# Kernel tuning notes

Measured on AMD Instinct MI355X. Metric: run time of the kernel, lower is better.

The kernel has to match this reference:

```python
import jax, jax.numpy as jnp
import numpy as np

M, N, K = 4096, 8192, 4096


def setup_inputs() -> dict:
    key = jax.random.key(0)
    k1, k2, k3, k4 = jax.random.split(key, 4)
    a = jax.random.randint(k1, (M, K), 0, 127, dtype=jnp.int32)  # int8 activations
    b = jax.random.randint(k2, (N, K), 0, 127, dtype=jnp.int32)  # int8 weights (row-major [N,K])
    alpha_row = jax.random.uniform(k3, (M, 1), dtype=jnp.float16)  # per-row dequant scale
    alpha_col = jax.random.uniform(k4, (1, N), dtype=jnp.float16)  # per-col dequant scale
    return {"a": a, "b": b, "alpha_row": alpha_row, "alpha_col": alpha_col}


def reference(a, b, alpha_row, alpha_col):
    # x = a @ b.T in fp32 (int8 values upcast), then rescale by outer product of scales
    x = jnp.matmul(a.astype(jnp.float32), b.astype(jnp.float32).T)  # [M, N]
    scale = alpha_row.astype(jnp.float32) * alpha_col.astype(jnp.float32)  # [M, N] via broadcast
    out = x * scale
    return out.astype(jnp.float16)
```

## Files before the change

kernel.cpp:

```cpp
#include <hip/hip_runtime.h>
#include <cstdint>
#include <cstddef>

#define M_DIM 4096
#define N_DIM 8192
#define K_DIM 4096

typedef __attribute__((ext_vector_type(4))) int int4v;

__global__ void __launch_bounds__(256) pack_frag(const int* __restrict__ a,
                                                 const int* __restrict__ b,
                                                 unsigned char* __restrict__ pa,
                                                 unsigned char* __restrict__ pb) {
    size_t t = (size_t)blockIdx.x * 256 + threadIdx.x;
    const size_t NA = (size_t)(M_DIM / 16) * (K_DIM / 64) * 64;
    const int* __restrict__ src;
    unsigned char* __restrict__ dst;
    if (t < NA) {
        src = a; dst = pa;
    } else {
        src = b; dst = pb; t -= NA;
    }
    const int l = (int)(t & 63);
    const int s = (int)((t >> 6) & 63);
    const int p = (int)(t >> 12);
    const int* g = src + ((size_t)(16 * p + (l & 15))) * K_DIM + s * 64 + (l >> 4) * 16;
    const int4v* g4 = (const int4v*)g;
    int4v o;
#pragma unroll
    for (int q = 0; q < 4; ++q) {
        int4v v = g4[q];
        o[q] = (v[0] & 0xff) | ((v[1] & 0xff) << 8) | ((v[2] & 0xff) << 16) | (v[3] << 24);
    }
    ((int4v*)dst)[t] = o;
}

__device__ inline void async_copy16(const unsigned char* g, unsigned char* l) {
    __builtin_amdgcn_global_load_lds(
        (const __attribute__((address_space(1))) void*)g,
        (__attribute__((address_space(3))) void*)l,
        16, 0, 0);
}

__global__ void __launch_bounds__(256) gemm_i8(const unsigned char* __restrict__ Ap,
                                               const unsigned char* __restrict__ Bp,
                                               const _Float16* __restrict__ arow,
                                               const _Float16* __restrict__ acol,
                                               _Float16* __restrict__ Cout) {
    __shared__ __align__(16) unsigned char Bs[16384];

    const int tid  = threadIdx.x;
    const int lane = tid & 63;
    const int wave = tid >> 6;
    const int bn   = blockIdx.x;
    const int bm   = blockIdx.y;

    const int wm = (wave & 1) * 64;
    const int wn = (wave >> 1) * 64;

    const unsigned char* Abase =
        Ap + ((size_t)(bm * 8 + (wm >> 4))) * 65536 + lane * 16;

    const size_t Bblk = (size_t)bn * 8 * 65536;
    const unsigned char* bg[4];
    unsigned char* bl[4];
#pragma unroll
    for (int r = 0; r < 4; ++r) {
        const int offu = r * 4096 + wave * 1024;
        bg[r] = Bp + Bblk + (size_t)(offu >> 11) * 65536 + (offu & 2047) + lane * 16;
        bl[r] = Bs + offu;
    }

    const int bf_base = ((wn >> 4) << 11) + lane * 16;

    int4v acc[4][4];
#pragma unroll
    for (int i = 0; i < 4; ++i)
#pragma unroll
        for (int j = 0; j < 4; ++j) acc[i][j] = (int4v)0;

    for (int T = 0; T < K_DIM / 128; ++T) {
        const int gk = T * 2048;

        int4v af[2][4];
#pragma unroll
        for (int h = 0; h < 2; ++h)
#pragma unroll
            for (int i = 0; i < 4; ++i)
                af[h][i] = *(const int4v*)(Abase + (size_t)i * 65536 + gk + h * 1024);

#pragma unroll
        for (int r = 0; r < 4; ++r) async_copy16(bg[r] + gk, bl[r]);
        __syncthreads();

#pragma unroll
        for (int h = 0; h < 2; ++h) {
            int4v bf[4];
#pragma unroll
            for (int j = 0; j < 4; ++j)
                bf[j] = *(const int4v*)(Bs + bf_base + j * 2048 + h * 1024);
#pragma unroll
            for (int i = 0; i < 4; ++i)
#pragma unroll
                for (int j = 0; j < 4; ++j)
                    acc[i][j] = __builtin_amdgcn_mfma_i32_16x16x64_i8(af[h][i], bf[j],
                                                                      acc[i][j], 0, 0, 0);
        }
        __syncthreads();
    }

    const int gcol0 = bn * 128 + wn + (lane & 15);
    float ac4[4];
#pragma unroll
    for (int j = 0; j < 4; ++j) ac4[j] = (float)acol[gcol0 + j * 16];

    const size_t grow0 = (size_t)bm * 128 + wm + (lane >> 4) * 4;
#pragma unroll
    for (int i = 0; i < 4; ++i) {
#pragma unroll
        for (int r = 0; r < 4; ++r) {
            const size_t row = grow0 + i * 16 + r;
            const float ar = (float)arow[row];
            _Float16* outp = Cout + row * (size_t)N_DIM + gcol0;
#pragma unroll
            for (int j = 0; j < 4; ++j) {
                float v = (float)acc[i][j][r] * ar * ac4[j];
                outp[j * 16] = (_Float16)v;
            }
        }
    }
}

extern "C" void kernel_launch(void* const* d_in, const int* in_sizes, int n_in,
                              void* d_out, int out_size, void* d_ws, size_t ws_size,
                              hipStream_t stream) {
    const int* a = (const int*)d_in[0];
    const int* b = (const int*)d_in[1];
    const _Float16* ar = (const _Float16*)d_in[2];
    const _Float16* ac = (const _Float16*)d_in[3];
    _Float16* out = (_Float16*)d_out;

    unsigned char* pa = (unsigned char*)d_ws;
    unsigned char* pb = pa + (size_t)M_DIM * K_DIM;

    const size_t total_frag = (size_t)(M_DIM / 16 + N_DIM / 16) * (K_DIM / 64) * 64;
    pack_frag<<<(int)(total_frag / 256), 256, 0, stream>>>(a, b, pa, pb);

    dim3 grid(N_DIM / 128, M_DIM / 128);
    gemm_i8<<<grid, 256, 0, stream>>>(pa, pb, ar, ac, out);
}
```

Before: 392.8 us.

## Double-buffer B tile in LDS, enlarge M tile to 256, coalesce pack kernel

The GEMM now double-buffers the B tile in LDS, prefetching the next K-slice with async global-to-LDS copies while computing on the current one. This drops one barrier per iteration. Each wave computes 128x64 instead of 64x64, which doubles A-register reuse of B fragments, and the grid is swapped so blockIdx.x walks M. The pack kernel is rewritten so each thread reads one coalesced 16-byte group and scatters a 4-byte word into the fragment layout. The larger accumulator array raises register pressure, and launch_bounds(256,2) limits occupancy.

```diff
diff --git a/kernel.cpp b/kernel.cpp
--- a/kernel.cpp
+++ b/kernel.cpp
@@ -13,7 +13,7 @@
                                                  unsigned char* __restrict__ pa,
                                                  unsigned char* __restrict__ pb) {
     size_t t = (size_t)blockIdx.x * 256 + threadIdx.x;
-    const size_t NA = (size_t)(M_DIM / 16) * (K_DIM / 64) * 64;
+    const size_t NA = (size_t)M_DIM * (K_DIM / 4);
     const int* __restrict__ src;
     unsigned char* __restrict__ dst;
     if (t < NA) {
@@ -21,18 +21,14 @@
     } else {
         src = b; dst = pb; t -= NA;
     }
-    const int l = (int)(t & 63);
-    const int s = (int)((t >> 6) & 63);
-    const int p = (int)(t >> 12);
-    const int* g = src + ((size_t)(16 * p + (l & 15))) * K_DIM + s * 64 + (l >> 4) * 16;
-    const int4v* g4 = (const int4v*)g;
-    int4v o;
-#pragma unroll
-    for (int q = 0; q < 4; ++q) {
-        int4v v = g4[q];
-        o[q] = (v[0] & 0xff) | ((v[1] & 0xff) << 8) | ((v[2] & 0xff) << 16) | (v[3] << 24);
-    }
-    ((int4v*)dst)[t] = o;
+    const int r = (int)(t >> 10);
+    const int g = (int)(t & 1023);
+    int4v v = *(const int4v*)(src + (size_t)r * K_DIM + 4 * g);
+    const int w = (v[0] & 0xff) | ((v[1] & 0xff) << 8) | ((v[2] & 0xff) << 16) | (v[3] << 24);
+    const int p = r >> 4, lr = r & 15;
+    const int s = g >> 4, q = (g >> 2) & 3, bo = (g & 3) * 4;
+    const size_t off = ((size_t)(p * 64 + s) * 64 + (lr + 16 * q)) * 16 + bo;
+    *(int*)(dst + off) = w;
 }
 
 __device__ inline void async_copy16(const unsigned char* g, unsigned char* l) {
@@ -42,65 +38,71 @@
         16, 0, 0);
 }
 
-__global__ void __launch_bounds__(256) gemm_i8(const unsigned char* __restrict__ Ap,
-                                               const unsigned char* __restrict__ Bp,
-                                               const _Float16* __restrict__ arow,
-                                               const _Float16* __restrict__ acol,
-                                               _Float16* __restrict__ Cout) {
-    __shared__ __align__(16) unsigned char Bs[16384];
+__global__ void __launch_bounds__(256, 2) gemm_i8(const unsigned char* __restrict__ Ap,
+                                                  const unsigned char* __restrict__ Bp,
+                                                  const _Float16* __restrict__ arow,
+                                                  const _Float16* __restrict__ acol,
+                                                  _Float16* __restrict__ Cout) {
+    __shared__ __align__(16) unsigned char Bs[2 * 16384];
 
     const int tid  = threadIdx.x;
     const int lane = tid & 63;
     const int wave = tid >> 6;
-    const int bn   = blockIdx.x;
-    const int bm   = blockIdx.y;
+    const int bm   = blockIdx.x;
+    const int bn   = blockIdx.y;
 
-    const int wm = (wave & 1) * 64;
-    const int wn = (wave >> 1) * 64;
+    const int wmp = (wave & 1) * 8;
+    const int wnp = (wave >> 1) * 4;
 
-    const unsigned char* Abase =
-        Ap + ((size_t)(bm * 8 + (wm >> 4))) * 65536 + lane * 16;
+    const unsigned char* Abase = Ap + (size_t)(bm * 16 + wmp) * 65536 + lane * 16;
 
     const size_t Bblk = (size_t)bn * 8 * 65536;
     const unsigned char* bg[4];
-    unsigned char* bl[4];
+    int blo[4];
 #pragma unroll
     for (int r = 0; r < 4; ++r) {
         const int offu = r * 4096 + wave * 1024;
-        bg[r] = Bp + Bblk + (size_t)(offu >> 11) * 65536 + (offu & 2047) + lane * 16;
-        bl[r] = Bs + offu;
+        bg[r]  = Bp + Bblk + (size_t)(offu >> 11) * 65536 + (offu & 2047) + lane * 16;
+        blo[r] = offu;
     }
+    const int bf_base = wnp * 2048 + lane * 16;
 
-    const int bf_base = ((wn >> 4) << 11) + lane * 16;
-
-    int4v acc[4][4];
+    int4v acc[8][4];
 #pragma unroll
-    for (int i = 0; i < 4; ++i)
+    for (int i = 0; i < 8; ++i)
 #pragma unroll
         for (int j = 0; j < 4; ++j) acc[i][j] = (int4v)0;
 
+#pragma unroll
+    for (int r = 0; r < 4; ++r) async_copy16(bg[r], Bs + blo[r]);
+    __syncthreads();
+
     for (int T = 0; T < K_DIM / 128; ++T) {
-        const int gk = T * 2048;
+        const int cur = (T & 1) * 16384;
+        const int nxt = 16384 - cur;
+        const int gk  = T * 2048;
 
-        int4v af[2][4];
+        int4v af[2][8];
 #pragma unroll
         for (int h = 0; h < 2; ++h)
 #pragma unroll
-            for (int i = 0; i < 4; ++i)
+            for (int i = 0; i < 8; ++i)
                 af[h][i] = *(const int4v*)(Abase + (size_t)i * 65536 + gk + h * 1024);
 
+        if (T < K_DIM / 128 - 1) {
 #pragma unroll
-        for (int r = 0; r < 4; ++r) async_copy16(bg[r] + gk, bl[r]);
-        __syncthreads();
+            for (int r = 0; r < 4; ++r)
+                async_copy16(bg[r] + gk + 2048, Bs + nxt + blo[r]);
+        }
 
 #pragma unroll
         for (int h = 0; h < 2; ++h) {
             int4v bf[4];
 #pragma unroll
             for (int j = 0; j < 4; ++j)
-                bf[j] = *(const int4v*)(Bs + bf_base + j * 2048 + h * 1024);
+                bf[j] = *(const int4v*)(Bs + cur + bf_base + j * 2048 + h * 1024);
 #pragma unroll
-            for (int i = 0; i < 4; ++i)
+            for (int i = 0; i < 8; ++i)
 #pragma unroll
                 for (int j = 0; j < 4; ++j)
                     acc[i][j] = __builtin_amdgcn_mfma_i32_16x16x64_i8(af[h][i], bf[j],
@@ -109,14 +111,14 @@
         __syncthreads();
     }
 
-    const int gcol0 = bn * 128 + wn + (lane & 15);
+    const int gcol0 = bn * 128 + wnp * 16 + (lane & 15);
     float ac4[4];
 #pragma unroll
     for (int j = 0; j < 4; ++j) ac4[j] = (float)acol[gcol0 + j * 16];
 
-    const size_t grow0 = (size_t)bm * 128 + wm + (lane >> 4) * 4;
+    const size_t grow0 = (size_t)bm * 256 + wmp * 16 + (lane >> 4) * 4;
 #pragma unroll
-    for (int i = 0; i < 4; ++i) {
+    for (int i = 0; i < 8; ++i) {
 #pragma unroll
         for (int r = 0; r < 4; ++r) {
             const size_t row = grow0 + i * 16 + r;
@@ -143,9 +145,9 @@
     unsigned char* pa = (unsigned char*)d_ws;
     unsigned char* pb = pa + (size_t)M_DIM * K_DIM;
 
-    const size_t total_frag = (size_t)(M_DIM / 16 + N_DIM / 16) * (K_DIM / 64) * 64;
-    pack_frag<<<(int)(total_frag / 256), 256, 0, stream>>>(a, b, pa, pb);
+    const size_t groups = ((size_t)M_DIM + N_DIM) * (K_DIM / 4);
+    pack_frag<<<(int)(groups / 256), 256, 0, stream>>>(a, b, pa, pb);
 
-    dim3 grid(N_DIM / 128, M_DIM / 128);
+    dim3 grid(M_DIM / 256, N_DIM / 128);
     gemm_i8<<<grid, 256, 0, stream>>>(pa, pb, ar, ac, out);
 }
```

After: 428.0 us. 8.9% more time.

## Double-buffer B tiles in LDS and prefetch A fragments one K-step ahead

Applied to the files above, without the earlier changes.

Doubles the LDS buffer for B and splits the A fragment registers into ping-pong halves. Each iteration now issues the next tile's A loads and async B copies before computing on the current tile, so global latency can overlap with MFMA work. It also drops one barrier per iteration and adds a launch_bounds occupancy hint of 2. The cost is more registers for the second A buffer and twice the LDS, which may lower occupancy or cause spills.

```diff
diff --git a/kernel.cpp b/kernel.cpp
--- a/kernel.cpp
+++ b/kernel.cpp
@@ -42,12 +42,12 @@
         16, 0, 0);
 }
 
-__global__ void __launch_bounds__(256) gemm_i8(const unsigned char* __restrict__ Ap,
-                                               const unsigned char* __restrict__ Bp,
-                                               const _Float16* __restrict__ arow,
-                                               const _Float16* __restrict__ acol,
-                                               _Float16* __restrict__ Cout) {
-    __shared__ __align__(16) unsigned char Bs[16384];
+__global__ void __launch_bounds__(256, 2) gemm_i8(const unsigned char* __restrict__ Ap,
+                                                  const unsigned char* __restrict__ Bp,
+                                                  const _Float16* __restrict__ arow,
+                                                  const _Float16* __restrict__ acol,
+                                                  _Float16* __restrict__ Cout) {
+    __shared__ __align__(16) unsigned char Bs[2 * 16384];
 
     const int tid  = threadIdx.x;
     const int lane = tid & 63;
@@ -58,19 +58,17 @@
     const int wm = (wave & 1) * 64;
     const int wn = (wave >> 1) * 64;
 
-    const unsigned char* Abase =
-        Ap + ((size_t)(bm * 8 + (wm >> 4))) * 65536 + lane * 16;
+    const unsigned char* Abase = Ap + (size_t)(bm * 8 + (wm >> 4)) * 65536 + lane * 16;
 
     const size_t Bblk = (size_t)bn * 8 * 65536;
     const unsigned char* bg[4];
-    unsigned char* bl[4];
+    int blo[4];
 #pragma unroll
     for (int r = 0; r < 4; ++r) {
         const int offu = r * 4096 + wave * 1024;
-        bg[r] = Bp + Bblk + (size_t)(offu >> 11) * 65536 + (offu & 2047) + lane * 16;
-        bl[r] = Bs + offu;
+        bg[r]  = Bp + Bblk + (size_t)(offu >> 11) * 65536 + (offu & 2047) + lane * 16;
+        blo[r] = offu;
     }
-
     const int bf_base = ((wn >> 4) << 11) + lane * 16;
 
     int4v acc[4][4];
@@ -79,31 +77,47 @@
 #pragma unroll
         for (int j = 0; j < 4; ++j) acc[i][j] = (int4v)0;
 
-    for (int T = 0; T < K_DIM / 128; ++T) {
-        const int gk = T * 2048;
-
-        int4v af[2][4];
-#pragma unroll
-        for (int h = 0; h < 2; ++h)
-#pragma unroll
-            for (int i = 0; i < 4; ++i)
-                af[h][i] = *(const int4v*)(Abase + (size_t)i * 65536 + gk + h * 1024);
+    const int NT = K_DIM / 128;
+    int4v af[2][2][4];
 
 #pragma unroll
-        for (int r = 0; r < 4; ++r) async_copy16(bg[r] + gk, bl[r]);
-        __syncthreads();
+    for (int h = 0; h < 2; ++h)
+#pragma unroll
+        for (int i = 0; i < 4; ++i)
+            af[0][h][i] = *(const int4v*)(Abase + (size_t)i * 65536 + h * 1024);
+#pragma unroll
+    for (int r = 0; r < 4; ++r) async_copy16(bg[r], Bs + blo[r]);
+    __syncthreads();
 
+#pragma unroll 2
+    for (int T = 0; T < NT; ++T) {
+        const int pp = T & 1;
+        const int gkn = (T + 1) * 2048;
+
+        if (T + 1 < NT) {
+#pragma unroll
+            for (int h = 0; h < 2; ++h)
+#pragma unroll
+                for (int i = 0; i < 4; ++i)
+                    af[pp ^ 1][h][i] =
+                        *(const int4v*)(Abase + (size_t)i * 65536 + gkn + h * 1024);
+#pragma unroll
+            for (int r = 0; r < 4; ++r)
+                async_copy16(bg[r] + gkn, Bs + (pp ^ 1) * 16384 + blo[r]);
+        }
+
+        const unsigned char* Bcur = Bs + pp * 16384;
 #pragma unroll
         for (int h = 0; h < 2; ++h) {
             int4v bf[4];
 #pragma unroll
             for (int j = 0; j < 4; ++j)
-                bf[j] = *(const int4v*)(Bs + bf_base + j * 2048 + h * 1024);
+                bf[j] = *(const int4v*)(Bcur + bf_base + j * 2048 + h * 1024);
 #pragma unroll
             for (int i = 0; i < 4; ++i)
 #pragma unroll
                 for (int j = 0; j < 4; ++j)
-                    acc[i][j] = __builtin_amdgcn_mfma_i32_16x16x64_i8(af[h][i], bf[j],
+                    acc[i][j] = __builtin_amdgcn_mfma_i32_16x16x64_i8(af[pp][h][i], bf[j],
                                                                       acc[i][j], 0, 0, 0);
         }
         __syncthreads();
```

Measured after the change: 401.5 us. 2.2% more time.

## Use 256x256 block tiles with double-buffered LDS staging for A and B

Applied to the files above, without the earlier changes.

Grows the block tile from 128x128 to 256x256 with 512 threads (8 waves, each 64x128 output). A is now staged through LDS like B, and both use double-buffered async global-to-LDS copies so the next K-slice loads while the current one computes. The intent is to raise arithmetic intensity, cut redundant global traffic, and overlap memory with MFMA work. The cost is more accumulator registers (128 VGPRs of acc) and 64KB of LDS per block, which may limit occupancy. The grid drops to 512 blocks, which could leave the wave tail uneven across CUs.

```diff
diff --git a/kernel.cpp b/kernel.cpp
--- a/kernel.cpp
+++ b/kernel.cpp
@@ -42,12 +42,13 @@
         16, 0, 0);
 }
 
-__global__ void __launch_bounds__(256) gemm_i8(const unsigned char* __restrict__ Ap,
-                                               const unsigned char* __restrict__ Bp,
-                                               const _Float16* __restrict__ arow,
-                                               const _Float16* __restrict__ acol,
-                                               _Float16* __restrict__ Cout) {
-    __shared__ __align__(16) unsigned char Bs[16384];
+__global__ void __launch_bounds__(512, 2) gemm_i8(const unsigned char* __restrict__ Ap,
+                                                  const unsigned char* __restrict__ Bp,
+                                                  const _Float16* __restrict__ arow,
+                                                  const _Float16* __restrict__ acol,
+                                                  _Float16* __restrict__ Cout) {
+    __shared__ __align__(16) unsigned char As[2 * 16384];
+    __shared__ __align__(16) unsigned char Bs[2 * 16384];
 
     const int tid  = threadIdx.x;
     const int lane = tid & 63;
@@ -55,66 +56,76 @@
     const int bn   = blockIdx.x;
     const int bm   = blockIdx.y;
 
-    const int wm = (wave & 1) * 64;
-    const int wn = (wave >> 1) * 64;
+    const int pm0 = (wave & 3) * 4;
+    const int pn0 = (wave >> 2) * 8;
 
-    const unsigned char* Abase =
-        Ap + ((size_t)(bm * 8 + (wm >> 4))) * 65536 + lane * 16;
-
-    const size_t Bblk = (size_t)bn * 8 * 65536;
-    const unsigned char* bg[4];
-    unsigned char* bl[4];
+    const unsigned char* ag[2];
+    const unsigned char* bg[2];
+    int slo[2];
 #pragma unroll
-    for (int r = 0; r < 4; ++r) {
-        const int offu = r * 4096 + wave * 1024;
-        bg[r] = Bp + Bblk + (size_t)(offu >> 11) * 65536 + (offu & 2047) + lane * 16;
-        bl[r] = Bs + offu;
+    for (int r = 0; r < 2; ++r) {
+        const int p = 2 * wave + r;
+        ag[r]  = Ap + ((size_t)(bm * 16 + p) * 64) * 1024 + lane * 16;
+        bg[r]  = Bp + ((size_t)(bn * 16 + p) * 64) * 1024 + lane * 16;
+        slo[r] = p * 1024;
     }
 
-    const int bf_base = ((wn >> 4) << 11) + lane * 16;
+    const int a_off = pm0 * 1024 + lane * 16;
+    const int b_off = pn0 * 1024 + lane * 16;
 
-    int4v acc[4][4];
+    int4v acc[4][8];
 #pragma unroll
     for (int i = 0; i < 4; ++i)
 #pragma unroll
-        for (int j = 0; j < 4; ++j) acc[i][j] = (int4v)0;
+        for (int j = 0; j < 8; ++j) acc[i][j] = (int4v)0;
 
-    for (int T = 0; T < K_DIM / 128; ++T) {
-        const int gk = T * 2048;
-
-        int4v af[2][4];
-#pragma unroll
-        for (int h = 0; h < 2; ++h)
-#pragma unroll
-            for (int i = 0; i < 4; ++i)
-                af[h][i] = *(const int4v*)(Abase + (size_t)i * 65536 + gk + h * 1024);
+    const int NT = K_DIM / 64;
 
 #pragma unroll
-        for (int r = 0; r < 4; ++r) async_copy16(bg[r] + gk, bl[r]);
-        __syncthreads();
+    for (int r = 0; r < 2; ++r) {
+        async_copy16(ag[r], As + slo[r]);
+        async_copy16(bg[r], Bs + slo[r]);
+    }
+    __syncthreads();
+
+#pragma unroll 2
+    for (int T = 0; T < NT; ++T) {
+        const int cur = (T & 1) * 16384;
+        const int nxt = cur ^ 16384;
+
+        if (T + 1 < NT) {
+            const size_t gko = (size_t)(T + 1) * 1024;
+#pragma unroll
+            for (int r = 0; r < 2; ++r) {
+                async_copy16(ag[r] + gko, As + nxt + slo[r]);
+                async_copy16(bg[r] + gko, Bs + nxt + slo[r]);
+            }
+        }
+
+        int4v af[4], bf[8];
+#pragma unroll
+        for (int i = 0; i < 4; ++i)
+            af[i] = *(const int4v*)(As + cur + a_off + i * 1024);
+#pragma unroll
+        for (int j = 0; j < 8; ++j)
+            bf[j] = *(const int4v*)(Bs + cur + b_off + j * 1024);
 
 #pragma unroll
-        for (int h = 0; h < 2; ++h) {
-            int4v bf[4];
+        for (int i = 0; i < 4; ++i)
 #pragma unroll
-            for (int j = 0; j < 4; ++j)
-                bf[j] = *(const int4v*)(Bs + bf_base + j * 2048 + h * 1024);
-#pragma unroll
-            for (int i = 0; i < 4; ++i)
-#pragma unroll
-                for (int j = 0; j < 4; ++j)
-                    acc[i][j] = __builtin_amdgcn_mfma_i32_16x16x64_i8(af[h][i], bf[j],
-                                                                      acc[i][j], 0, 0, 0);
-        }
+            for (int j = 0; j < 8; ++j)
+                acc[i][j] = __builtin_amdgcn_mfma_i32_16x16x64_i8(af[i], bf[j],
+                                                                  acc[i][j], 0, 0, 0);
+
         __syncthreads();
     }
 
-    const int gcol0 = bn * 128 + wn + (lane & 15);
-    float ac4[4];
+    const int gcol0 = bn * 256 + pn0 * 16 + (lane & 15);
+    float ac8[8];
 #pragma unroll
-    for (int j = 0; j < 4; ++j) ac4[j] = (float)acol[gcol0 + j * 16];
+    for (int j = 0; j < 8; ++j) ac8[j] = (float)acol[gcol0 + j * 16];
 
-    const size_t grow0 = (size_t)bm * 128 + wm + (lane >> 4) * 4;
+    const size_t grow0 = (size_t)bm * 256 + pm0 * 16 + (lane >> 4) * 4;
 #pragma unroll
     for (int i = 0; i < 4; ++i) {
 #pragma unroll
@@ -123,8 +134,8 @@
             const float ar = (float)arow[row];
             _Float16* outp = Cout + row * (size_t)N_DIM + gcol0;
 #pragma unroll
-            for (int j = 0; j < 4; ++j) {
-                float v = (float)acc[i][j][r] * ar * ac4[j];
+            for (int j = 0; j < 8; ++j) {
+                float v = (float)acc[i][j][r] * ar * ac8[j];
                 outp[j * 16] = (_Float16)v;
             }
         }
@@ -146,6 +157,6 @@
     const size_t total_frag = (size_t)(M_DIM / 16 + N_DIM / 16) * (K_DIM / 64) * 64;
     pack_frag<<<(int)(total_frag / 256), 256, 0, stream>>>(a, b, pa, pb);
 
-    dim3 grid(N_DIM / 128, M_DIM / 128);
-    gemm_i8<<<grid, 256, 0, stream>>>(pa, pb, ar, ac, out);
+    dim3 grid(N_DIM / 256, M_DIM / 256);
+    gemm_i8<<<grid, 512, 0, stream>>>(pa, pb, ar, ac, out);
 }
```

Result: faster. 382.4 us (-2.6%).
